# Optimization experiments

Measured on AMD Instinct MI355X. Metric: run time of the kernel, lower is better.

Reference implementation:

```python
import jax, jax.numpy as jnp
import numpy as np

INPUT_DIM = 1024
UNITS = 1024

def setup_inputs() -> dict:
    key = jax.random.key(0)
    ks = jax.random.split(key, 7)
    B, S = 4, 2048
    x = jax.random.normal(ks[0], (B, S, INPUT_DIM), dtype=jnp.float32)
    # nn.Linear weights stored as [out, in]; biases [out]
    scale = 1.0 / np.sqrt(INPUT_DIM)
    Wq = jax.random.uniform(ks[1], (UNITS, INPUT_DIM), jnp.float32, -scale, scale)
    bq = jax.random.uniform(ks[2], (UNITS,), jnp.float32, -scale, scale)
    Wk = jax.random.uniform(ks[3], (UNITS, INPUT_DIM), jnp.float32, -scale, scale)
    bk = jax.random.uniform(ks[4], (UNITS,), jnp.float32, -scale, scale)
    Wv = jax.random.uniform(ks[5], (UNITS, INPUT_DIM), jnp.float32, -scale, scale)
    bv = jax.random.uniform(ks[6], (UNITS,), jnp.float32, -scale, scale)
    return {"x": x, "Wq": Wq, "bq": bq, "Wk": Wk, "bk": bk, "Wv": Wv, "bv": bv}

def reference(x, Wq, bq, Wk, bk, Wv, bv):
    # Q/K/V projections: [B,S,D] @ [D,U]
    Q = jnp.einsum('bsd,ud->bsu', x, Wq) + bq
    K = jnp.einsum('bsd,ud->bsu', x, Wk) + bk
    V = jnp.einsum('bsd,ud->bsu', x, Wv) + bv
    scores = jnp.einsum('bqu,bku->bqk', Q, K) / jnp.sqrt(jnp.float32(UNITS))
    attn = jax.nn.softmax(scores, axis=-1)
    return jnp.einsum('bqk,bku->bqu', attn, V)
```

## Files before the change

kernel.cpp:

```cpp
#include <hip/hip_runtime.h>
#include <cstdint>
#include <cstddef>


typedef unsigned short ushort_t;
typedef __attribute__((ext_vector_type(8))) short short8;
typedef __attribute__((ext_vector_type(4))) float f32x4;

#define AS1 __attribute__((address_space(1)))
#define AS3 __attribute__((address_space(3)))

__device__ __forceinline__ ushort_t f2bf(float f) {
    unsigned int u = __float_as_uint(f);
    u += 0x7FFFu + ((u >> 16) & 1u);
    return (ushort_t)(u >> 16);
}
__device__ __forceinline__ float bf2f(ushort_t b) {
    return __uint_as_float(((unsigned)b) << 16);
}

__device__ __forceinline__ void async_ld16(const void* g, unsigned lds_off) {
    __builtin_amdgcn_global_load_lds((const AS1 void*)(uintptr_t)g,
                                     (AS3 void*)(uintptr_t)lds_off,
                                     16, 0, 0);
}

template <typename OT, int EPI, int NB, int BK>
__global__ __launch_bounds__(256, 2) void gemm_bt(
    const ushort_t* __restrict__ A, const ushort_t* __restrict__ B0,
    const ushort_t* __restrict__ B1,
    const float* __restrict__ bias0, const float* __restrict__ bias1,
    OT* __restrict__ C0, OT* __restrict__ C1,
    int K, int lda, int ldb, int ldc, float scale,
    long long aOffZ, long long bOffZ, long long cOffZ)
{
    constexpr int P     = BK / 8;
    constexpr int NCALL = BK / 16;
    constexpr int RPC   = 2048 / BK;

    __shared__ __align__(16) ushort_t As[128 * BK];
    __shared__ __align__(16) ushort_t Bs[NB][128 * BK];
    __shared__ float rs[128];

    const int tid  = threadIdx.x;
    const int wave = tid >> 6;
    const int lane = tid & 63;

    A  += (size_t)blockIdx.z * aOffZ;
    B0 += (size_t)blockIdx.z * bOffZ;
    if (NB == 2) B1 += (size_t)blockIdx.z * bOffZ;

    const int m0 = blockIdx.y * 128;
    const int n0 = blockIdx.x * 128;
    const int wm = (wave >> 1) * 64;
    const int wn = (wave & 1) * 64;

    const unsigned ldsA  = (unsigned)(uintptr_t)&As[0];
    const unsigned ldsB0 = (unsigned)(uintptr_t)&Bs[0][0];
    const unsigned ldsB1 = (NB == 2) ? (unsigned)(uintptr_t)&Bs[NB - 1][0] : 0;

    const int srow = wave * (RPC / 4) + lane / P;
    const int cd   = ((lane & (P - 1)) - srow) & (P - 1);
    const ushort_t* gA  = A  + (size_t)(m0 + srow) * lda + cd * 8;
    const ushort_t* gB0 = B0 + (size_t)(n0 + srow) * ldb + cd * 8;
    const ushort_t* gB1 = (NB == 2) ? B1 + (size_t)(n0 + srow) * ldb + cd * 8
                                    : nullptr;
    const unsigned lw = (wave << 10);

    const int frow = lane & 15;
    const int fg   = lane >> 4;

    f32x4 acc[NB][4][4] = {};
    float rsacc[4] = {0.f, 0.f, 0.f, 0.f};

    for (int k0 = 0; k0 < K; k0 += BK) {
        if (k0) __syncthreads();
#pragma unroll
        for (int c = 0; c < NCALL; ++c) {
            const size_t ro = (size_t)c * RPC;
            async_ld16(gA + ro * lda, ldsA + c * 4096 + lw);
            async_ld16(gB0 + ro * ldb, ldsB0 + c * 4096 + lw);
            if (NB == 2) async_ld16(gB1 + ro * ldb, ldsB1 + c * 4096 + lw);
        }
        gA += BK; gB0 += BK; if (NB == 2) gB1 += BK;
        __syncthreads();

#pragma unroll
        for (int t = 0; t < BK / 32; ++t) {
            const int pa = (((t << 2) + fg + frow) & (P - 1)) << 3;
            short8 af[4], bf[4];
#pragma unroll
            for (int i = 0; i < 4; ++i)
                af[i] = *(const short8*)&As[(wm + i * 16 + frow) * BK + pa];
            if (EPI == 4 && wn == 0) {
#pragma unroll
                for (int i = 0; i < 4; ++i)
#pragma unroll
                    for (int e = 0; e < 8; ++e)
                        rsacc[i] += bf2f((ushort_t)af[i][e]);
            }
#pragma unroll
            for (int j = 0; j < 4; ++j)
                bf[j] = *(const short8*)&Bs[0][(wn + j * 16 + frow) * BK + pa];
#pragma unroll
            for (int i = 0; i < 4; ++i)
#pragma unroll
                for (int j = 0; j < 4; ++j)
                    acc[0][i][j] = __builtin_amdgcn_mfma_f32_16x16x32_bf16(
                        af[i], bf[j], acc[0][i][j], 0, 0, 0);
            if (NB == 2) {
#pragma unroll
                for (int j = 0; j < 4; ++j)
                    bf[j] = *(const short8*)&Bs[NB - 1][(wn + j * 16 + frow) * BK + pa];
#pragma unroll
                for (int i = 0; i < 4; ++i)
#pragma unroll
                    for (int j = 0; j < 4; ++j)
                        acc[NB - 1][i][j] = __builtin_amdgcn_mfma_f32_16x16x32_bf16(
                            af[i], bf[j], acc[NB - 1][i][j], 0, 0, 0);
            }
        }
    }

    if (EPI == 4) {
        if (wn == 0) {
#pragma unroll
            for (int i = 0; i < 4; ++i) {
                float s = rsacc[i];
                s += __shfl_xor(s, 16, 64);
                s += __shfl_xor(s, 32, 64);
                rs[wm + i * 16 + frow] = s;
            }
        }
        __syncthreads();
    }

    const int r0 = (lane >> 4) << 2;
    const int c0 = lane & 15;
#pragma unroll
    for (int o = 0; o < NB; ++o) {
        OT* C = (o == 0) ? C0 : C1;
        C += (size_t)blockIdx.z * cOffZ;
        const float* bia = (o == 0) ? bias0 : bias1;
#pragma unroll
        for (int i = 0; i < 4; ++i) {
            float bm[4];
            if (EPI == 2) {
#pragma unroll
                for (int r = 0; r < 4; ++r)
                    bm[r] = bias0[m0 + wm + i * 16 + r0 + r];
            }
            if (EPI == 4) {
#pragma unroll
                for (int r = 0; r < 4; ++r)
                    bm[r] = 1.0f / rs[wm + i * 16 + r0 + r];
            }
#pragma unroll
            for (int j = 0; j < 4; ++j) {
                const int n = n0 + wn + j * 16 + c0;
                const float bn = (EPI == 1) ? bia[n] : 0.f;
#pragma unroll
                for (int r = 0; r < 4; ++r) {
                    const int m = m0 + wm + i * 16 + r0 + r;
                    float v = acc[o][i][j][r] * scale;
                    if (EPI == 1) v += bn;
                    if (EPI == 2) v += bm[r];
                    if (EPI == 3) v = __expf(v);
                    if (EPI == 4) v *= bm[r];
                    if constexpr (sizeof(OT) == 2)
                        C[(size_t)m * ldc + n] = f2bf(v);
                    else
                        C[(size_t)m * ldc + n] = v;
                }
            }
        }
    }
}

__global__ __launch_bounds__(256) void cvt_all(
    const float* __restrict__ x,  const float* __restrict__ wq,
    const float* __restrict__ wk, const float* __restrict__ wv,
    ushort_t* __restrict__ xb,  ushort_t* __restrict__ wqb,
    ushort_t* __restrict__ wkb, ushort_t* __restrict__ wvb)
{
    const int b = blockIdx.x;
    const float* src; ushort_t* dst; size_t base;
    if (b < 4096)      { src = x;  dst = xb;  base = (size_t)b * 2048; }
    else if (b < 4608) { src = wq; dst = wqb; base = (size_t)(b - 4096) * 2048; }
    else if (b < 5120) { src = wk; dst = wkb; base = (size_t)(b - 4608) * 2048; }
    else               { src = wv; dst = wvb; base = (size_t)(b - 5120) * 2048; }
    const size_t i = base + threadIdx.x * 8;
    const f32x4 a = *(const f32x4*)(src + i);
    const f32x4 c = *(const f32x4*)(src + i + 4);
    short8 o;
    o[0] = (short)f2bf(a[0]); o[1] = (short)f2bf(a[1]);
    o[2] = (short)f2bf(a[2]); o[3] = (short)f2bf(a[3]);
    o[4] = (short)f2bf(c[0]); o[5] = (short)f2bf(c[1]);
    o[6] = (short)f2bf(c[2]); o[7] = (short)f2bf(c[3]);
    *(short8*)(dst + i) = o;
}

extern "C" void kernel_launch(void* const* d_in, const int* in_sizes, int n_in,
                              void* d_out, int out_size, void* d_ws, size_t ws_size,
                              hipStream_t stream)
{
    const float* x  = (const float*)d_in[0];
    const float* Wq = (const float*)d_in[1];
    const float* bq = (const float*)d_in[2];
    const float* Wk = (const float*)d_in[3];
    const float* bk = (const float*)d_in[4];
    const float* Wv = (const float*)d_in[5];
    const float* bv = (const float*)d_in[6];
    float* out = (float*)d_out;

    char* ws = (char*)d_ws;
    const size_t MB = 1ull << 20;
    ushort_t* Xb  = (ushort_t*)(ws);
    ushort_t* Wqb = (ushort_t*)(ws + 16 * MB);
    ushort_t* Wkb = (ushort_t*)(ws + 18 * MB);
    ushort_t* Wvb = (ushort_t*)(ws + 20 * MB);
    ushort_t* Qb  = (ushort_t*)(ws + 32 * MB);
    ushort_t* Kb  = (ushort_t*)(ws + 48 * MB);
    ushort_t* Vt  = (ushort_t*)(ws + 64 * MB);
    ushort_t* Sc  = (ushort_t*)(ws);

    cvt_all<<<dim3(5632), dim3(256), 0, stream>>>(
        x, Wq, Wk, Wv, Xb, Wqb, Wkb, Wvb);

    gemm_bt<ushort_t, 1, 2, 64><<<dim3(8, 64, 1), dim3(256), 0, stream>>>(
        Xb, Wqb, Wkb, bq, bk, Qb, Kb, 1024, 1024, 1024, 1024, 1.0f, 0, 0, 0);

    gemm_bt<ushort_t, 2, 1, 64><<<dim3(64, 8, 1), dim3(256), 0, stream>>>(
        Wvb, Xb, nullptr, bv, nullptr, Vt, nullptr,
        1024, 1024, 1024, 8192, 1.0f, 0, 0, 0);

    gemm_bt<ushort_t, 3, 1, 64><<<dim3(16, 16, 4), dim3(256), 0, stream>>>(
        Qb, Kb, nullptr, nullptr, nullptr, Sc, nullptr,
        1024, 1024, 1024, 2048, 0.03125f,
        2048ll * 1024, 2048ll * 1024, 2048ll * 2048);

    gemm_bt<float, 4, 1, 64><<<dim3(8, 16, 4), dim3(256), 0, stream>>>(
        Sc, Vt, nullptr, nullptr, nullptr, out, nullptr,
        2048, 2048, 8192, 1024, 1.0f,
        2048ll * 2048, 2048ll, 2048ll * 1024);
}
```

Measured before the change: 240.7 us.

## Replace GEMM with 8-wave 256-row double-buffered pipelined kernel, merge QK weights

Replaces the 4-wave 128x128 single-buffered GEMM with an 8-wave kernel using 256-row tiles (256 or 128 columns) and double-buffered LDS. Async global-to-LDS loads for the next tiles are interleaved with MFMA phases, using explicit vmcnt waits and raised wave priority around the matrix ops. Wq and Wk are treated as one contiguous 2048-row weight matrix so Q and K come out of a single fused output buffer. This aims to hide load latency and improve data reuse per tile. It costs more LDS and registers per block and gives fewer blocks per grid, which may hurt occupancy and tail balance.

```diff
diff --git a/kernel.cpp b/kernel.cpp
--- a/kernel.cpp
+++ b/kernel.cpp
@@ -25,107 +25,160 @@
                                      16, 0, 0);
 }
 
-template <typename OT, int EPI, int NB, int BK>
-__global__ __launch_bounds__(256, 2) void gemm_bt(
-    const ushort_t* __restrict__ A, const ushort_t* __restrict__ B0,
-    const ushort_t* __restrict__ B1,
+template <int N>
+__device__ __forceinline__ void wait_vmcnt() {
+    if constexpr (N == 0)      asm volatile("s_waitcnt vmcnt(0)" ::: "memory");
+    else if constexpr (N == 4) asm volatile("s_waitcnt vmcnt(4)" ::: "memory");
+    else                       asm volatile("s_waitcnt vmcnt(6)" ::: "memory");
+}
+
+template <typename OT, int EPI, int BN>
+__global__ __launch_bounds__(512, 2) void gemm8(
+    const ushort_t* __restrict__ A, const ushort_t* __restrict__ B,
     const float* __restrict__ bias0, const float* __restrict__ bias1,
-    OT* __restrict__ C0, OT* __restrict__ C1,
-    int K, int lda, int ldb, int ldc, float scale,
+    OT* __restrict__ C, int K, int lda, int ldb, int ldc, float scale,
     long long aOffZ, long long bOffZ, long long cOffZ)
 {
-    constexpr int P     = BK / 8;
-    constexpr int NCALL = BK / 16;
-    constexpr int RPC   = 2048 / BK;
-
-    __shared__ __align__(16) ushort_t As[128 * BK];
-    __shared__ __align__(16) ushort_t Bs[NB][128 * BK];
-    __shared__ float rs[128];
+    constexpr int NJ   = BN / 64;
+    constexpr int NBH  = (BN == 256) ? 2 : 1;
+    constexpr int VPRO = (BN == 256) ? 6 : 4;
+
+    __shared__ __align__(16) ushort_t As[2][2][128 * 64];
+    __shared__ __align__(16) ushort_t Bs[2][NBH][128 * 64];
+    __shared__ float rs[256];
 
     const int tid  = threadIdx.x;
     const int wave = tid >> 6;
     const int lane = tid & 63;
 
-    A  += (size_t)blockIdx.z * aOffZ;
-    B0 += (size_t)blockIdx.z * bOffZ;
-    if (NB == 2) B1 += (size_t)blockIdx.z * bOffZ;
-
-    const int m0 = blockIdx.y * 128;
-    const int n0 = blockIdx.x * 128;
-    const int wm = (wave >> 1) * 64;
-    const int wn = (wave & 1) * 64;
-
-    const unsigned ldsA  = (unsigned)(uintptr_t)&As[0];
-    const unsigned ldsB0 = (unsigned)(uintptr_t)&Bs[0][0];
-    const unsigned ldsB1 = (NB == 2) ? (unsigned)(uintptr_t)&Bs[NB - 1][0] : 0;
-
-    const int srow = wave * (RPC / 4) + lane / P;
-    const int cd   = ((lane & (P - 1)) - srow) & (P - 1);
-    const ushort_t* gA  = A  + (size_t)(m0 + srow) * lda + cd * 8;
-    const ushort_t* gB0 = B0 + (size_t)(n0 + srow) * ldb + cd * 8;
-    const ushort_t* gB1 = (NB == 2) ? B1 + (size_t)(n0 + srow) * ldb + cd * 8
-                                    : nullptr;
-    const unsigned lw = (wave << 10);
+    A += (size_t)blockIdx.z * aOffZ;
+    B += (size_t)blockIdx.z * bOffZ;
+
+    const int m0 = blockIdx.y * 256;
+    const int n0 = blockIdx.x * BN;
+    const int g  = wave >> 2;
+    const int wm = g * 128;
+    const int wn = (wave & 3) * (BN / 4);
+
+    const int srow = wave * 8 + (lane >> 3);
+    const int cd   = ((lane & 7) - srow) & 7;
+    const unsigned lw = (unsigned)(wave << 10);
+
+    const ushort_t* Ast = A + (size_t)(m0 + srow) * lda + cd * 8;
+    const ushort_t* Bst = B + (size_t)(n0 + srow) * ldb + cd * 8;
+
+    unsigned aB[2][2], bB[2][NBH];
+#pragma unroll
+    for (int b2 = 0; b2 < 2; ++b2) {
+        aB[b2][0] = (unsigned)(uintptr_t)&As[b2][0][0];
+        aB[b2][1] = (unsigned)(uintptr_t)&As[b2][1][0];
+#pragma unroll
+        for (int h = 0; h < NBH; ++h)
+            bB[b2][h] = (unsigned)(uintptr_t)&Bs[b2][h][0];
+    }
+
+    auto stA = [&](int t, int rsel) {
+        const int buf = t & 1;
+        const int k0  = t << 6;
+        async_ld16(Ast + (size_t)(rsel * 64) * lda + k0,
+                   aB[buf][0] + (unsigned)(rsel * 8192) + lw);
+        async_ld16(Ast + (size_t)(rsel * 64 + 128) * lda + k0,
+                   aB[buf][1] + (unsigned)(rsel * 8192) + lw);
+    };
+    auto stB = [&](int t, int h) {
+        const int buf = t & 1;
+        const int k0  = t << 6;
+        async_ld16(Bst + (size_t)(h * 128) * ldb + k0, bB[buf][h] + lw);
+        async_ld16(Bst + (size_t)(h * 128 + 64) * ldb + k0,
+                   bB[buf][h] + 8192 + lw);
+    };
 
     const int frow = lane & 15;
     const int fg   = lane >> 4;
-
-    f32x4 acc[NB][4][4] = {};
-    float rsacc[4] = {0.f, 0.f, 0.f, 0.f};
-
-    for (int k0 = 0; k0 < K; k0 += BK) {
-        if (k0) __syncthreads();
-#pragma unroll
-        for (int c = 0; c < NCALL; ++c) {
-            const size_t ro = (size_t)c * RPC;
-            async_ld16(gA + ro * lda, ldsA + c * 4096 + lw);
-            async_ld16(gB0 + ro * ldb, ldsB0 + c * 4096 + lw);
-            if (NB == 2) async_ld16(gB1 + ro * ldb, ldsB1 + c * 4096 + lw);
-        }
-        gA += BK; gB0 += BK; if (NB == 2) gB1 += BK;
-        __syncthreads();
-
-#pragma unroll
-        for (int t = 0; t < BK / 32; ++t) {
-            const int pa = (((t << 2) + fg + frow) & (P - 1)) << 3;
-            short8 af[4], bf[4];
-#pragma unroll
-            for (int i = 0; i < 4; ++i)
-                af[i] = *(const short8*)&As[(wm + i * 16 + frow) * BK + pa];
+    const int hB   = (BN == 256) ? (wn >> 7) : 0;
+
+    const int NT = K >> 6;
+
+    f32x4 acc[8][NJ] = {};
+    float rsacc[8] = {};
+    short8 bfr[NJ][2];
+
+    stB(0, 0);
+    if (BN == 256) stB(0, 1);
+    stA(0, 0); stA(0, 1);
+    stB(1, 0);
+    if (BN == 256) stB(1, 1);
+    stA(1, 0);
+    wait_vmcnt<VPRO>();
+    __builtin_amdgcn_s_barrier();
+
+    for (int t = 0; t < NT; ++t) {
+        const int buf = t & 1;
+        const ushort_t* Aw = &As[buf][g][0];
+        const ushort_t* Bw = &Bs[buf][hB][0];
+#pragma unroll
+        for (int ph = 0; ph < 4; ++ph) {
+            short8 af[2][2];
+#pragma unroll
+            for (int di = 0; di < 2; ++di) {
+                const int r = (ph * 2 + di) * 16 + frow;
+#pragma unroll
+                for (int kk = 0; kk < 2; ++kk)
+                    af[di][kk] = *(const short8*)
+                        &Aw[r * 64 + (((kk << 2) + fg + r) & 7) * 8];
+            }
+            if (ph == 0) {
+#pragma unroll
+                for (int j = 0; j < NJ; ++j) {
+                    const int rb = (wn & 127) + j * 16 + frow;
+#pragma unroll
+                    for (int kk = 0; kk < 2; ++kk)
+                        bfr[j][kk] = *(const short8*)
+                            &Bw[rb * 64 + (((kk << 2) + fg + rb) & 7) * 8];
+                }
+                if (t + 1 < NT) stA(t + 1, 1);
+            }
+            if (ph == 1 && t + 2 < NT) stB(t + 2, 0);
+            if (ph == 2 && t + 2 < NT) {
+                if (BN == 256) stB(t + 2, 1);
+                else           stA(t + 2, 0);
+            }
+            if (ph == 3) {
+                if (BN == 256 && t + 2 < NT) stA(t + 2, 0);
+                if (t + 2 < NT)      wait_vmcnt<VPRO>();
+                else if (t + 1 < NT) wait_vmcnt<0>();
+            }
+            __builtin_amdgcn_s_barrier();
+            asm volatile("s_waitcnt lgkmcnt(0)" ::: "memory");
+            __builtin_amdgcn_s_setprio(1);
+#pragma unroll
+            for (int di = 0; di < 2; ++di)
+#pragma unroll
+                for (int j = 0; j < NJ; ++j)
+#pragma unroll
+                    for (int kk = 0; kk < 2; ++kk)
+                        acc[ph * 2 + di][j] =
+                            __builtin_amdgcn_mfma_f32_16x16x32_bf16(
+                                af[di][kk], bfr[j][kk],
+                                acc[ph * 2 + di][j], 0, 0, 0);
+            __builtin_amdgcn_s_setprio(0);
             if (EPI == 4 && wn == 0) {
 #pragma unroll
-                for (int i = 0; i < 4; ++i)
-#pragma unroll
-                    for (int e = 0; e < 8; ++e)
-                        rsacc[i] += bf2f((ushort_t)af[i][e]);
-            }
-#pragma unroll
-            for (int j = 0; j < 4; ++j)
-                bf[j] = *(const short8*)&Bs[0][(wn + j * 16 + frow) * BK + pa];
-#pragma unroll
-            for (int i = 0; i < 4; ++i)
-#pragma unroll
-                for (int j = 0; j < 4; ++j)
-                    acc[0][i][j] = __builtin_amdgcn_mfma_f32_16x16x32_bf16(
-                        af[i], bf[j], acc[0][i][j], 0, 0, 0);
-            if (NB == 2) {
-#pragma unroll
-                for (int j = 0; j < 4; ++j)
-                    bf[j] = *(const short8*)&Bs[NB - 1][(wn + j * 16 + frow) * BK + pa];
-#pragma unroll
-                for (int i = 0; i < 4; ++i)
-#pragma unroll
-                    for (int j = 0; j < 4; ++j)
-                        acc[NB - 1][i][j] = __builtin_amdgcn_mfma_f32_16x16x32_bf16(
-                            af[i], bf[j], acc[NB - 1][i][j], 0, 0, 0);
-            }
+                for (int di = 0; di < 2; ++di)
+#pragma unroll
+                    for (int kk = 0; kk < 2; ++kk)
+#pragma unroll
+                        for (int e = 0; e < 8; ++e)
+                            rsacc[ph * 2 + di] += bf2f((ushort_t)af[di][kk][e]);
+            }
+            __builtin_amdgcn_s_barrier();
         }
     }
 
     if (EPI == 4) {
         if (wn == 0) {
 #pragma unroll
-            for (int i = 0; i < 4; ++i) {
+            for (int i = 0; i < 8; ++i) {
                 float s = rsacc[i];
                 s += __shfl_xor(s, 16, 64);
                 s += __shfl_xor(s, 32, 64);
@@ -135,43 +188,39 @@
         __syncthreads();
     }
 
-    const int r0 = (lane >> 4) << 2;
+    C += (size_t)blockIdx.z * cOffZ;
+    const int r0 = fg << 2;
     const int c0 = lane & 15;
 #pragma unroll
-    for (int o = 0; o < NB; ++o) {
-        OT* C = (o == 0) ? C0 : C1;
-        C += (size_t)blockIdx.z * cOffZ;
-        const float* bia = (o == 0) ? bias0 : bias1;
-#pragma unroll
-        for (int i = 0; i < 4; ++i) {
-            float bm[4];
-            if (EPI == 2) {
-#pragma unroll
-                for (int r = 0; r < 4; ++r)
-                    bm[r] = bias0[m0 + wm + i * 16 + r0 + r];
-            }
-            if (EPI == 4) {
-#pragma unroll
-                for (int r = 0; r < 4; ++r)
-                    bm[r] = 1.0f / rs[wm + i * 16 + r0 + r];
-            }
-#pragma unroll
-            for (int j = 0; j < 4; ++j) {
-                const int n = n0 + wn + j * 16 + c0;
-                const float bn = (EPI == 1) ? bia[n] : 0.f;
-#pragma unroll
-                for (int r = 0; r < 4; ++r) {
-                    const int m = m0 + wm + i * 16 + r0 + r;
-                    float v = acc[o][i][j][r] * scale;
-                    if (EPI == 1) v += bn;
-                    if (EPI == 2) v += bm[r];
-                    if (EPI == 3) v = __expf(v);
-                    if (EPI == 4) v *= bm[r];
-                    if constexpr (sizeof(OT) == 2)
-                        C[(size_t)m * ldc + n] = f2bf(v);
-                    else
-                        C[(size_t)m * ldc + n] = v;
-                }
+    for (int i = 0; i < 8; ++i) {
+        float bm[4];
+        if (EPI == 2) {
+#pragma unroll
+            for (int r = 0; r < 4; ++r)
+                bm[r] = bias0[m0 + wm + i * 16 + r0 + r];
+        }
+        if (EPI == 4) {
+#pragma unroll
+            for (int r = 0; r < 4; ++r)
+                bm[r] = 1.0f / rs[wm + i * 16 + r0 + r];
+        }
+#pragma unroll
+        for (int j = 0; j < NJ; ++j) {
+            const int n = n0 + wn + j * 16 + c0;
+            float bn = 0.f;
+            if (EPI == 1) bn = (n < 1024) ? bias0[n] : bias1[n - 1024];
+#pragma unroll
+            for (int r = 0; r < 4; ++r) {
+                const int m = m0 + wm + i * 16 + r0 + r;
+                float v = acc[i][j][r] * scale;
+                if (EPI == 1) v += bn;
+                if (EPI == 2) v += bm[r];
+                if (EPI == 3) v = __expf(v);
+                if (EPI == 4) v *= bm[r];
+                if constexpr (sizeof(OT) == 2)
+                    C[(size_t)m * ldc + n] = f2bf(v);
+                else
+                    C[(size_t)m * ldc + n] = v;
             }
         }
     }
@@ -215,32 +264,28 @@
 
     char* ws = (char*)d_ws;
     const size_t MB = 1ull << 20;
-    ushort_t* Xb  = (ushort_t*)(ws);
-    ushort_t* Wqb = (ushort_t*)(ws + 16 * MB);
-    ushort_t* Wkb = (ushort_t*)(ws + 18 * MB);
-    ushort_t* Wvb = (ushort_t*)(ws + 20 * MB);
-    ushort_t* Qb  = (ushort_t*)(ws + 32 * MB);
-    ushort_t* Kb  = (ushort_t*)(ws + 48 * MB);
-    ushort_t* Vt  = (ushort_t*)(ws + 64 * MB);
-    ushort_t* Sc  = (ushort_t*)(ws);
+    ushort_t* Xb   = (ushort_t*)(ws);
+    ushort_t* Wqkb = (ushort_t*)(ws + 16 * MB);
+    ushort_t* Wkb  = (ushort_t*)(ws + 18 * MB);
+    ushort_t* Wvb  = (ushort_t*)(ws + 20 * MB);
+    ushort_t* QKb  = (ushort_t*)(ws + 32 * MB);
+    ushort_t* Vt   = (ushort_t*)(ws + 64 * MB);
+    ushort_t* Sc   = (ushort_t*)(ws);
 
     cvt_all<<<dim3(5632), dim3(256), 0, stream>>>(
-        x, Wq, Wk, Wv, Xb, Wqb, Wkb, Wvb);
-
-    gemm_bt<ushort_t, 1, 2, 64><<<dim3(8, 64, 1), dim3(256), 0, stream>>>(
-        Xb, Wqb, Wkb, bq, bk, Qb, Kb, 1024, 1024, 1024, 1024, 1.0f, 0, 0, 0);
-
-    gemm_bt<ushort_t, 2, 1, 64><<<dim3(64, 8, 1), dim3(256), 0, stream>>>(
-        Wvb, Xb, nullptr, bv, nullptr, Vt, nullptr,
-        1024, 1024, 1024, 8192, 1.0f, 0, 0, 0);
-
-    gemm_bt<ushort_t, 3, 1, 64><<<dim3(16, 16, 4), dim3(256), 0, stream>>>(
-        Qb, Kb, nullptr, nullptr, nullptr, Sc, nullptr,
-        1024, 1024, 1024, 2048, 0.03125f,
-        2048ll * 1024, 2048ll * 1024, 2048ll * 2048);
-
-    gemm_bt<float, 4, 1, 64><<<dim3(8, 16, 4), dim3(256), 0, stream>>>(
-        Sc, Vt, nullptr, nullptr, nullptr, out, nullptr,
-        2048, 2048, 8192, 1024, 1.0f,
+        x, Wq, Wk, Wv, Xb, Wqkb, Wkb, Wvb);
+
+    gemm8<ushort_t, 1, 256><<<dim3(8, 32, 1), dim3(512), 0, stream>>>(
+        Xb, Wqkb, bq, bk, QKb, 1024, 1024, 1024, 2048, 1.0f, 0, 0, 0);
+
+    gemm8<ushort_t, 2, 128><<<dim3(64, 4, 1), dim3(512), 0, stream>>>(
+        Wvb, Xb, bv, nullptr, Vt, 1024, 1024, 1024, 8192, 1.0f, 0, 0, 0);
+
+    gemm8<ushort_t, 3, 256><<<dim3(8, 8, 4), dim3(512), 0, stream>>>(
+        QKb, QKb + 1024, nullptr, nullptr, Sc, 1024, 2048, 2048, 2048,
+        0.03125f, 2048ll * 2048, 2048ll * 2048, 2048ll * 2048);
+
+    gemm8<float, 4, 128><<<dim3(8, 8, 4), dim3(512), 0, stream>>>(
+        Sc, Vt, nullptr, nullptr, out, 2048, 2048, 8192, 1024, 1.0f,
         2048ll * 2048, 2048ll, 2048ll * 1024);
 }
```

Measured after the change: 259.5 us. 1.08x slower.
